# Performance work log

Hardware: AMD Instinct MI355X
Metric: run time of the kernel (lower is better)

The kernel has to match this reference:

```python
import jax, jax.numpy as jnp
import numpy as np

B, C, H, W = 8, 2, 256, 256


def edt2d(mask):
    """Exact Euclidean distance transform, scipy.ndimage.distance_transform_edt semantics:
    for nonzero (True) pixels, distance to the nearest zero pixel. mask: bool [B,H,W]."""
    b, h, w = mask.shape
    INF = jnp.float32(1e4)  # larger than any achievable in-image distance
    m = jnp.moveaxis(mask, 1, 0)  # [H,B,W]

    def step(carry, mm):
        d = jnp.where(mm, carry + 1.0, 0.0)
        return d, d

    init = jnp.full((b, w), INF, jnp.float32)
    _, fwd = jax.lax.scan(step, init, m)            # top-down 1D column distance
    _, bwd = jax.lax.scan(step, init, m[::-1])      # bottom-up
    g = jnp.minimum(fwd, bwd[::-1])                 # [H,B,W] vertical nearest-zero distance
    g2 = jnp.moveaxis(g, 0, 1) ** 2                 # [B,H,W]

    j = jnp.arange(w, dtype=jnp.float32)
    D2 = (j[:, None] - j[None, :]) ** 2             # [W,W] horizontal squared offsets

    def per_image(gi):                              # gi: [H,W] squared column distances
        # d[i,j] = sqrt(min_k g2[i,k] + (j-k)^2)  -- exact separable EDT
        return jnp.sqrt(jnp.min(gi[:, None, :] + D2[None, :, :], axis=-1))

    return jax.lax.map(per_image, g2)               # sequence over batch to bound memory


def setup_inputs() -> dict:
    key = jax.random.key(0)
    k1, k2 = jax.random.split(key)
    preds = jax.random.normal(k1, (B, C, H, W), dtype=jnp.float32)
    target = jax.random.randint(k2, (B, H, W), 0, 2, dtype=jnp.int32)
    return {"preds": preds, "target": target}


def reference(preds, target):
    # ignore_index handling: replace 255 with target.min() (no-op when 255 absent)
    tmin = target.min()
    target = jnp.where(target == 255, tmin, target)
    gt = target.astype(jnp.float32)

    # softmax then argmax over class dim (== argmax of logits)
    pc = jnp.argmax(jax.nn.softmax(preds, axis=1), axis=1).astype(jnp.float32)  # [B,H,W]

    # EDT(pos) + EDT(neg), done under no_grad in the original
    pc_dist = jax.lax.stop_gradient(edt2d(pc > 0) + edt2d(pc == 0))
    gt_dist = jax.lax.stop_gradient(edt2d(gt > 0) + edt2d(gt == 0))

    pred_error = jnp.abs(gt - pc)                   # sqrt((gt-pc)^2)
    dist = jnp.sqrt(pc_dist ** 2 + gt_dist ** 2)
    multipled = jnp.sqrt(pred_error * dist + 1e-9)
    return multipled.mean()
```

## Files before the change

### kernel.cpp

```cpp
#include <hip/hip_runtime.h>
#include <cfloat>

#define BB 8
#define CC 2
#define HH 256
#define WW 256

typedef unsigned long long ull;

static constexpr float EDT_INF = 1e4f;
static constexpr int   NPIX    = BB * HH * WW;

__device__ __forceinline__ float hdist2(const ull* zm, int pos) {
    float fwd = EDT_INF + (float)(pos + 1);
    {
        int k = pos - 1;
        if (k >= 0) {
            int w = k >> 6;
            ull t = zm[w] & (~0ULL >> (63 - (k & 63)));
            for (;;) {
                if (t) { int j = (w << 6) + 63 - __builtin_clzll(t); fwd = (float)(pos - j); break; }
                if (--w < 0) break;
                t = zm[w];
            }
        }
    }
    float bwd = EDT_INF + (float)(256 - pos);
    {
        int k = pos + 1;
        if (k < 256) {
            int w = k >> 6;
            ull t = zm[w] & (~0ULL << (k & 63));
            for (;;) {
                if (t) { int j = (w << 6) + __builtin_ctzll(t); bwd = (float)(j - pos); break; }
                if (++w >= 4) break;
                t = zm[w];
            }
        }
    }
    float g = fminf(fwd, bwd);
    return g * g;
}

__device__ __forceinline__ int nearest_set(const ull* zm, int pos) {
    int best = 1 << 20;
    {
        int k = pos - 1;
        if (k >= 0) {
            int w = k >> 6;
            ull t = zm[w] & (~0ULL >> (63 - (k & 63)));
            for (;;) {
                if (t) { int j = (w << 6) + 63 - __builtin_clzll(t); best = pos - j; break; }
                if (--w < 0) break;
                t = zm[w];
            }
        }
    }
    {
        int k = pos + 1;
        if (k < 256) {
            int w = k >> 6;
            ull t = zm[w] & (~0ULL << (k & 63));
            for (;;) {
                if (t) { int j = (w << 6) + __builtin_ctzll(t); best = min(best, j - pos); break; }
                if (++w >= 4) break;
                t = zm[w];
            }
        }
    }
    return best;
}

__global__ void k_masks(const float* __restrict__ preds,
                        const int*   __restrict__ target,
                        ull* __restrict__ mPC, ull* __restrict__ mGT0,
                        ull* __restrict__ mG255, int* __restrict__ tminPart) {
    const int blk = blockIdx.x;
    const int b  = blk >> 5;
    const int ig = blk & 31;
    const int wv = threadIdx.x >> 6;
    const int ln = threadIdx.x & 63;
    const int w  = (wv << 6) | ln;

    int tmin = 0x7fffffff;
#pragma unroll
    for (int r = 0; r < 8; ++r) {
        int i = ig * 8 + r;
        float a0 = preds[((size_t)b * CC + 0) * HH * WW + (size_t)i * WW + w];
        float a1 = preds[((size_t)b * CC + 1) * HH * WW + (size_t)i * WW + w];
        bool pc = (a1 > a0);
        int tv = target[((size_t)b * HH + i) * WW + w];
        tmin = min(tmin, tv);
        ull bp = __ballot(pc);
        ull b0 = __ballot(tv > 0);
        ull b2 = __ballot(tv == 255);
        if (ln == 0) {
            size_t midx = ((size_t)b * HH + i) * 4 + wv;
            mPC[midx] = bp; mGT0[midx] = b0; mG255[midx] = b2;
        }
    }
    for (int off = 32; off > 0; off >>= 1) tmin = min(tmin, __shfl_down(tmin, off));
    __shared__ int swv[4];
    if (ln == 0) swv[wv] = tmin;
    __syncthreads();
    if (threadIdx.x == 0)
        tminPart[blk] = min(min(swv[0], swv[1]), min(swv[2], swv[3]));
}

__global__ void k_fused(const int* __restrict__ target,
                        const ull* __restrict__ mPC,
                        const ull* __restrict__ mGT0,
                        const ull* __restrict__ mG255,
                        const int* __restrict__ tminPart,
                        float* __restrict__ partials) {
    const int blk = blockIdx.x;
    const int b = blk >> 8, j = blk & 255;
    const int i = threadIdx.x;
    const int wv = i >> 6, ln = i & 63;

    __shared__ int stw[4];
    {
        int v = tminPart[i];
        for (int off = 32; off > 0; off >>= 1) v = min(v, __shfl_down(v, off));
        if (ln == 0) stw[wv] = v;
    }
    __syncthreads();
    const int tmin = min(min(stw[0], stw[1]), min(stw[2], stw[3]));
    const bool allpos = (tmin > 0);

    ull wp[4], wg[4];
    {
        const ull* pP = mPC   + ((size_t)b * HH + i) * 4;
        const ull* p0 = mGT0  + ((size_t)b * HH + i) * 4;
        const ull* p2 = mG255 + ((size_t)b * HH + i) * 4;
#pragma unroll
        for (int k = 0; k < 4; ++k) {
            wp[k] = pP[k];
            ull g = p0[k];
            if (!allpos) g &= ~p2[k];
            wg[k] = g;
        }
    }
    const bool pc = (wp[j >> 6] >> (j & 63)) & 1ULL;
    const bool gt = (wg[j >> 6] >> (j & 63)) & 1ULL;

    ull zp[4], zg[4];
#pragma unroll
    for (int k = 0; k < 4; ++k) {
        zp[k] = pc ? ~wp[k] : wp[k];
        zg[k] = gt ? ~wg[k] : wg[k];
    }

    __shared__ float s_p[HH], s_g[HH];
    __shared__ ull cshP[4], cshG[4];
    s_p[i] = hdist2(zp, j);
    s_g[i] = hdist2(zg, j);
    {
        ull bp = __ballot(pc);
        ull bg = __ballot(gt);
        if (ln == 0) { cshP[wv] = bp; cshG[wv] = bg; }
    }
    __syncthreads();

    ull cp[4], cg[4];
#pragma unroll
    for (int k = 0; k < 4; ++k) {
        ull P = cshP[k], G = cshG[k];
        cp[k] = pc ? ~P : P;
        cg[k] = gt ? ~G : G;
    }
    const int dvp = nearest_set(cp, i);
    const int dvg = nearest_set(cg, i);

    float mn = s_p[i];
    {
        int dmax = min(dvp, HH);
        for (int d = 1; d < dmax; ++d) {
            float dd = (float)(d * d);
            if (dd >= mn) break;
            int kl = i - d, kr = i + d;
            if (kl >= 0) mn = fminf(mn, dd + s_p[kl]);
            if (kr < HH) mn = fminf(mn, dd + s_p[kr]);
        }
        float dv = (float)dvp;
        mn = fminf(mn, dv * dv);
    }
    float pd = sqrtf(mn);

    float mg = s_g[i];
    {
        int dmax = min(dvg, HH);
        for (int d = 1; d < dmax; ++d) {
            float dd = (float)(d * d);
            if (dd >= mg) break;
            int kl = i - d, kr = i + d;
            if (kl >= 0) mg = fminf(mg, dd + s_g[kl]);
            if (kr < HH) mg = fminf(mg, dd + s_g[kr]);
        }
        float dv = (float)dvg;
        mg = fminf(mg, dv * dv);
    }
    float gd = sqrtf(mg);

    int tv = target[((size_t)b * HH + i) * WW + j];
    if (tv == 255) tv = tmin;
    float gtv = (float)tv;
    float pcv = pc ? 1.0f : 0.0f;
    float err  = fabsf(gtv - pcv);
    float dist = sqrtf(pd * pd + gd * gd);
    float mult = sqrtf(err * dist + 1e-9f);

    __shared__ float sws[4];
    for (int off = 32; off > 0; off >>= 1) mult += __shfl_down(mult, off);
    if (ln == 0) sws[wv] = mult;
    __syncthreads();
    if (i == 0) partials[blk] = ((sws[0] + sws[1]) + sws[2]) + sws[3];
}

__global__ void k_final(const float* __restrict__ partials, float* __restrict__ out) {
    __shared__ float s[256];
    float acc = 0.0f;
    for (int k = threadIdx.x; k < BB * WW; k += 256) acc += partials[k];
    s[threadIdx.x] = acc;
    __syncthreads();
    for (int st = 128; st > 0; st >>= 1) {
        if (threadIdx.x < st) s[threadIdx.x] += s[threadIdx.x + st];
        __syncthreads();
    }
    if (threadIdx.x == 0) out[0] = s[0] * (1.0f / (float)NPIX);
}

extern "C" void kernel_launch(void* const* d_in, const int* in_sizes, int n_in,
                              void* d_out, int out_size, void* d_ws, size_t ws_size,
                              hipStream_t stream) {
    const float* preds  = (const float*)d_in[0];
    const int*   target = (const int*)d_in[1];
    float* out = (float*)d_out;

    ull* mPC   = (ull*)d_ws;
    ull* mGT0  = mPC  + (size_t)BB * HH * 4;
    ull* mG255 = mGT0 + (size_t)BB * HH * 4;
    float* partials = (float*)(mG255 + (size_t)BB * HH * 4);
    int*   tminPart = (int*)(partials + BB * WW);

    k_masks<<<256, 256, 0, stream>>>(preds, target, mPC, mGT0, mG255, tminPart);
    k_fused<<<BB * WW, HH, 0, stream>>>(target, mPC, mGT0, mG255, tminPart, partials);
    k_final<<<1, 256, 0, stream>>>(partials, out);
}
```

Baseline: 25.46 us.

## Process four columns per block and fuse final reduction via last-block atomic

Each fused block now handles four image columns, loading the row masks and the global tmin once instead of per column, which cuts the block count from 2048 to 512. The separate final-reduction kernel is removed: every block writes a partial sum and bumps an atomic counter, and the last block to finish reduces all partials. This saves one kernel launch and some redundant setup, at the cost of less parallelism per launch and a serial loop of four column passes with extra barriers. The counter is reset in the mask kernel.

```diff
diff --git a/kernel.cpp b/kernel.cpp
--- a/kernel.cpp
+++ b/kernel.cpp
@@ -10,6 +10,7 @@
 
 static constexpr float EDT_INF = 1e4f;
 static constexpr int   NPIX    = BB * HH * WW;
+#define FBLK 512
 
 __device__ __forceinline__ float hdist2(const ull* zm, int pos) {
     float fwd = EDT_INF + (float)(pos + 1);
@@ -74,13 +75,16 @@
 __global__ void k_masks(const float* __restrict__ preds,
                         const int*   __restrict__ target,
                         ull* __restrict__ mPC, ull* __restrict__ mGT0,
-                        ull* __restrict__ mG255, int* __restrict__ tminPart) {
+                        ull* __restrict__ mG255, int* __restrict__ tminPart,
+                        unsigned int* __restrict__ count) {
     const int blk = blockIdx.x;
     const int b  = blk >> 5;
     const int ig = blk & 31;
     const int wv = threadIdx.x >> 6;
     const int ln = threadIdx.x & 63;
     const int w  = (wv << 6) | ln;
+
+    if (blk == 0 && threadIdx.x == 0) *count = 0u;
 
     int tmin = 0x7fffffff;
 #pragma unroll
@@ -107,40 +111,11 @@
         tminPart[blk] = min(min(swv[0], swv[1]), min(swv[2], swv[3]));
 }
 
-__global__ void k_fused(const int* __restrict__ target,
-                        const ull* __restrict__ mPC,
-                        const ull* __restrict__ mGT0,
-                        const ull* __restrict__ mG255,
-                        const int* __restrict__ tminPart,
-                        float* __restrict__ partials) {
-    const int blk = blockIdx.x;
-    const int b = blk >> 8, j = blk & 255;
-    const int i = threadIdx.x;
+__device__ __forceinline__ float column_partial(
+        const int* __restrict__ target, int b, int j, int i, int tmin,
+        const ull wp[4], const ull wg[4],
+        float* s_p, float* s_g, ull* cshP, ull* cshG, float* sws) {
     const int wv = i >> 6, ln = i & 63;
-
-    __shared__ int stw[4];
-    {
-        int v = tminPart[i];
-        for (int off = 32; off > 0; off >>= 1) v = min(v, __shfl_down(v, off));
-        if (ln == 0) stw[wv] = v;
-    }
-    __syncthreads();
-    const int tmin = min(min(stw[0], stw[1]), min(stw[2], stw[3]));
-    const bool allpos = (tmin > 0);
-
-    ull wp[4], wg[4];
-    {
-        const ull* pP = mPC   + ((size_t)b * HH + i) * 4;
-        const ull* p0 = mGT0  + ((size_t)b * HH + i) * 4;
-        const ull* p2 = mG255 + ((size_t)b * HH + i) * 4;
-#pragma unroll
-        for (int k = 0; k < 4; ++k) {
-            wp[k] = pP[k];
-            ull g = p0[k];
-            if (!allpos) g &= ~p2[k];
-            wg[k] = g;
-        }
-    }
     const bool pc = (wp[j >> 6] >> (j & 63)) & 1ULL;
     const bool gt = (wg[j >> 6] >> (j & 63)) & 1ULL;
 
@@ -150,9 +125,6 @@
         zp[k] = pc ? ~wp[k] : wp[k];
         zg[k] = gt ? ~wg[k] : wg[k];
     }
-
-    __shared__ float s_p[HH], s_g[HH];
-    __shared__ ull cshP[4], cshG[4];
     s_p[i] = hdist2(zp, j);
     s_g[i] = hdist2(zg, j);
     {
@@ -162,15 +134,15 @@
     }
     __syncthreads();
 
-    ull cp[4], cg[4];
+    ull cp[4], cgm[4];
 #pragma unroll
     for (int k = 0; k < 4; ++k) {
         ull P = cshP[k], G = cshG[k];
-        cp[k] = pc ? ~P : P;
-        cg[k] = gt ? ~G : G;
+        cp[k]  = pc ? ~P : P;
+        cgm[k] = gt ? ~G : G;
     }
     const int dvp = nearest_set(cp, i);
-    const int dvg = nearest_set(cg, i);
+    const int dvg = nearest_set(cgm, i);
 
     float mn = s_p[i];
     {
@@ -210,24 +182,84 @@
     float dist = sqrtf(pd * pd + gd * gd);
     float mult = sqrtf(err * dist + 1e-9f);
 
-    __shared__ float sws[4];
     for (int off = 32; off > 0; off >>= 1) mult += __shfl_down(mult, off);
     if (ln == 0) sws[wv] = mult;
     __syncthreads();
-    if (i == 0) partials[blk] = ((sws[0] + sws[1]) + sws[2]) + sws[3];
-}
-
-__global__ void k_final(const float* __restrict__ partials, float* __restrict__ out) {
-    __shared__ float s[256];
-    float acc = 0.0f;
-    for (int k = threadIdx.x; k < BB * WW; k += 256) acc += partials[k];
-    s[threadIdx.x] = acc;
-    __syncthreads();
-    for (int st = 128; st > 0; st >>= 1) {
-        if (threadIdx.x < st) s[threadIdx.x] += s[threadIdx.x + st];
+    return ((sws[0] + sws[1]) + sws[2]) + sws[3];
+}
+
+__global__ void __launch_bounds__(256)
+k_fused(const int* __restrict__ target,
+        const ull* __restrict__ mPC,
+        const ull* __restrict__ mGT0,
+        const ull* __restrict__ mG255,
+        const int* __restrict__ tminPart,
+        float* __restrict__ partialB,
+        unsigned int* __restrict__ count,
+        float* __restrict__ out) {
+    const int blk = blockIdx.x;
+    const int b = blk >> 6, jg = blk & 63;
+    const int i = threadIdx.x;
+    const int wv = i >> 6, ln = i & 63;
+
+    __shared__ float s_p[HH], s_g[HH];
+    __shared__ ull   cshP[4], cshG[4];
+    __shared__ int   stw[4];
+    __shared__ float sws[4];
+    __shared__ float sred[256];
+    __shared__ int   lastFlag;
+
+    {
+        int v = tminPart[i];
+        for (int off = 32; off > 0; off >>= 1) v = min(v, __shfl_down(v, off));
+        if (ln == 0) stw[wv] = v;
+    }
+    __syncthreads();
+    const int tmin = min(min(stw[0], stw[1]), min(stw[2], stw[3]));
+    const bool allpos = (tmin > 0);
+
+    ull wp[4], wg[4];
+    {
+        const ull* pP = mPC   + ((size_t)b * HH + i) * 4;
+        const ull* p0 = mGT0  + ((size_t)b * HH + i) * 4;
+        const ull* p2 = mG255 + ((size_t)b * HH + i) * 4;
+#pragma unroll
+        for (int k = 0; k < 4; ++k) {
+            wp[k] = pP[k];
+            ull g = p0[k];
+            if (!allpos) g &= ~p2[k];
+            wg[k] = g;
+        }
+    }
+
+    float bsum = 0.0f;
+    for (int c = 0; c < 4; ++c) {
+        const int j = jg * 4 + c;
+        float psum = column_partial(target, b, j, i, tmin, wp, wg,
+                                    s_p, s_g, cshP, cshG, sws);
+        bsum += psum;
         __syncthreads();
     }
-    if (threadIdx.x == 0) out[0] = s[0] * (1.0f / (float)NPIX);
+
+    if (i == 0) {
+        partialB[blk] = bsum;
+        __threadfence();
+        unsigned int old = atomicAdd(count, 1u);
+        lastFlag = (old == (unsigned int)(FBLK - 1)) ? 1 : 0;
+    }
+    __syncthreads();
+
+    if (lastFlag) {
+        __threadfence();
+        float acc = partialB[i] + partialB[i + 256];
+        sred[i] = acc;
+        __syncthreads();
+        for (int st = 128; st > 0; st >>= 1) {
+            if (i < st) sred[i] += sred[i + st];
+            __syncthreads();
+        }
+        if (i == 0) out[0] = sred[0] * (1.0f / (float)NPIX);
+    }
 }
 
 extern "C" void kernel_launch(void* const* d_in, const int* in_sizes, int n_in,
@@ -240,10 +272,12 @@
     ull* mPC   = (ull*)d_ws;
     ull* mGT0  = mPC  + (size_t)BB * HH * 4;
     ull* mG255 = mGT0 + (size_t)BB * HH * 4;
-    float* partials = (float*)(mG255 + (size_t)BB * HH * 4);
-    int*   tminPart = (int*)(partials + BB * WW);
-
-    k_masks<<<256, 256, 0, stream>>>(preds, target, mPC, mGT0, mG255, tminPart);
-    k_fused<<<BB * WW, HH, 0, stream>>>(target, mPC, mGT0, mG255, tminPart, partials);
-    k_final<<<1, 256, 0, stream>>>(partials, out);
-}
+    int*   tminPart = (int*)(mG255 + (size_t)BB * HH * 4);
+    float* partialB = (float*)(tminPart + 256);
+    unsigned int* count = (unsigned int*)(partialB + FBLK);
+
+    k_masks<<<256, 256, 0, stream>>>(preds, target, mPC, mGT0, mG255,
+                                     tminPart, count);
+    k_fused<<<FBLK, 256, 0, stream>>>(target, mPC, mGT0, mG255, tminPart,
+                                      partialB, count, out);
+}
```

After: 33.21 us. 1.3x slower.
